# Performance work log

Hardware: AMD Instinct MI355X
Metric: run time of the kernel (lower is better)

Reference implementation:

```python
import jax, jax.numpy as jnp
import numpy as np

D_MODEL = 1024
NUM_HEADS = 16
HEAD_DIM = D_MODEL // NUM_HEADS  # 64
B, S = 4, 2048


def setup_inputs() -> dict:
    key = jax.random.key(0)
    ks = jax.random.split(key, 10)
    scale = 1.0 / np.sqrt(D_MODEL)
    x = jax.random.normal(ks[0], (B, S, D_MODEL), dtype=jnp.float32)
    # per-head projection weights stacked over the head axis (matches ModuleList of Linears)
    Wq = jax.random.normal(ks[1], (NUM_HEADS, D_MODEL, HEAD_DIM), dtype=jnp.float32) * scale
    bq = jax.random.normal(ks[2], (NUM_HEADS, HEAD_DIM), dtype=jnp.float32) * 0.01
    Wk = jax.random.normal(ks[3], (NUM_HEADS, D_MODEL, HEAD_DIM), dtype=jnp.float32) * scale
    bk = jax.random.normal(ks[4], (NUM_HEADS, HEAD_DIM), dtype=jnp.float32) * 0.01
    Wv = jax.random.normal(ks[5], (NUM_HEADS, D_MODEL, HEAD_DIM), dtype=jnp.float32) * scale
    bv = jax.random.normal(ks[6], (NUM_HEADS, HEAD_DIM), dtype=jnp.float32) * 0.01
    Wo = jax.random.normal(ks[7], (D_MODEL, D_MODEL), dtype=jnp.float32) * scale
    bo = jax.random.normal(ks[8], (D_MODEL,), dtype=jnp.float32) * 0.01
    return {"hidden_state": x, "Wq": Wq, "bq": bq, "Wk": Wk, "bk": bk,
            "Wv": Wv, "bv": bv, "Wo": Wo, "bo": bo}


def reference(hidden_state, Wq, bq, Wk, bk, Wv, bv, Wo, bo):
    # q,k,v: [B, H, S, E]
    q = jnp.einsum('bsd,hde->bhse', hidden_state, Wq) + bq[None, :, None, :]
    k = jnp.einsum('bsd,hde->bhse', hidden_state, Wk) + bk[None, :, None, :]
    v = jnp.einsum('bsd,hde->bhse', hidden_state, Wv) + bv[None, :, None, :]
    scores = jnp.einsum('bhse,bhte->bhst', q, k) / jnp.sqrt(jnp.asarray(HEAD_DIM, q.dtype))
    weights = jax.nn.softmax(scores, axis=-1)  # [B, H, S, S]
    attn = jnp.einsum('bhst,bhte->bhse', weights, v)  # [B, H, S, E]
    # concat heads along feature dim (head order preserved)
    attn = jnp.transpose(attn, (0, 2, 1, 3)).reshape(hidden_state.shape[0], hidden_state.shape[1], D_MODEL)
    return attn @ Wo + bo
```

## Files before the change

### kernel.cpp

```cpp
#include <hip/hip_runtime.h>

typedef __bf16 bf16x8 __attribute__((ext_vector_type(8)));
typedef float f32x4 __attribute__((ext_vector_type(4)));
typedef unsigned int u32x4 __attribute__((ext_vector_type(4)));
typedef unsigned int u32x2 __attribute__((ext_vector_type(2)));
typedef unsigned short u16x8 __attribute__((ext_vector_type(8)));

#define MFMA_BF16(a, b, c) __builtin_amdgcn_mfma_f32_16x16x32_bf16((a), (b), (c), 0, 0, 0)

#define QSCALE 0.18033688011112043f

__device__ __forceinline__ unsigned short f2bf(float f) {
    unsigned int u = __builtin_bit_cast(unsigned int, f);
    u += 0x7FFFu + ((u >> 16) & 1u);
    return (unsigned short)(u >> 16);
}

__device__ __forceinline__ unsigned int pack_bf16_rne(float a, float b) {
    unsigned int ua = __builtin_bit_cast(unsigned int, a);
    unsigned int ub = __builtin_bit_cast(unsigned int, b);
    ua += 0x7FFFu + ((ua >> 16) & 1u);
    ub += 0x7FFFu + ((ub >> 16) & 1u);
    return __builtin_amdgcn_perm(ub, ua, 0x07060302);
}

#if __has_builtin(__builtin_amdgcn_cvt_pk_bf16_f32)
typedef __bf16 bf16x2 __attribute__((ext_vector_type(2)));
__device__ __forceinline__ unsigned int pack_bf16(float a, float b) {
    return __builtin_bit_cast(unsigned int, __builtin_amdgcn_cvt_pk_bf16_f32(a, b));
}
#else
__device__ __forceinline__ unsigned int pack_bf16(float a, float b) {
    return pack_bf16_rne(a, b);
}
#endif

#if __has_builtin(__builtin_amdgcn_exp2f)
__device__ __forceinline__ float fast_exp2(float x) { return __builtin_amdgcn_exp2f(x); }
#else
__device__ __forceinline__ float fast_exp2(float x) { return exp2f(x); }
#endif

__device__ __forceinline__ bf16x8 ldfrag(const unsigned short* p) {
    return __builtin_bit_cast(bf16x8, *(const u32x4*)p);
}

typedef const __attribute__((address_space(1))) void* gas_t;
typedef __attribute__((address_space(3))) void* las_t;
__device__ __forceinline__ void dma16(const unsigned short* g, unsigned short* l) {
    __builtin_amdgcn_global_load_lds((gas_t)(const void*)g, (las_t)(void*)l, 16, 0, 0);
}

__device__ __forceinline__ void pipeline_barrier() {
    __builtin_amdgcn_s_waitcnt(0);
    __syncthreads();
}


__global__ void cvt_x_kernel(const float* __restrict__ in, unsigned short* __restrict__ out) {
    long long t = (long long)blockIdx.x * 256 + threadIdx.x;
    const f32x4* p = (const f32x4*)in + t * 2;
    f32x4 v0 = p[0], v1 = p[1];
    u16x8 o;
    o[0] = f2bf(v0[0]); o[1] = f2bf(v0[1]); o[2] = f2bf(v0[2]); o[3] = f2bf(v0[3]);
    o[4] = f2bf(v1[0]); o[5] = f2bf(v1[1]); o[6] = f2bf(v1[2]); o[7] = f2bf(v1[3]);
    *((u16x8*)out + t) = o;
}

__global__ void cvt_wqkvT_kernel(const float* __restrict__ Wq, const float* __restrict__ Wk,
                                 const float* __restrict__ Wv, unsigned short* __restrict__ WT) {
    int n = blockIdx.x * 256 + threadIdx.x;
    int d0 = blockIdx.y * 8;
    int proj = n >> 10, rem = n & 1023, h = rem >> 6, e = rem & 63;
    const float* W = (proj == 0) ? Wq : (proj == 1) ? Wk : Wv;
    const float* src = W + (size_t)h * 65536 + (size_t)d0 * 64 + e;
    u16x8 o;
#pragma unroll
    for (int j = 0; j < 8; j++) o[j] = f2bf(src[j * 64]);
    *(u16x8*)(WT + (size_t)n * 1024 + d0) = o;
}

__global__ void cvt_woT_kernel(const float* __restrict__ Wo, unsigned short* __restrict__ WoT) {
    int n = blockIdx.x * 256 + threadIdx.x;
    int d0 = blockIdx.y * 8;
    const float* src = Wo + (size_t)d0 * 1024 + n;
    u16x8 o;
#pragma unroll
    for (int j = 0; j < 8; j++) o[j] = f2bf(src[j * 1024]);
    *(u16x8*)(WoT + (size_t)n * 1024 + d0) = o;
}


__global__ __launch_bounds__(256) void gemm_qkv_kernel(
    const unsigned short* __restrict__ A, const unsigned short* __restrict__ BT,
    const float* __restrict__ bq, const float* __restrict__ bk, const float* __restrict__ bv,
    unsigned short* __restrict__ Qo, unsigned short* __restrict__ Ko, unsigned short* __restrict__ VTo) {
    __shared__ unsigned short As[2 * 128 * 32];
    __shared__ unsigned short Bs[2 * 128 * 32];
    const int tid = threadIdx.x;
    const int m0 = blockIdx.y * 128, n0 = blockIdx.x * 128;
    const int w = tid >> 6, lane = tid & 63, lr = lane & 15, quad = lane >> 4;
    const int wy = w >> 1, wx = w & 1;
    f32x4 acc[4][4];
#pragma unroll
    for (int i = 0; i < 4; i++)
#pragma unroll
        for (int j = 0; j < 4; j++) acc[i][j] = (f32x4){0.f, 0.f, 0.f, 0.f};
    const int drow = lane >> 2;
    const int dchunk = (lane & 3) ^ (drow & 3);
    const unsigned short* gA = A + (size_t)(m0 + w * 32 + drow) * 1024 + dchunk * 8;
    const unsigned short* gB = BT + (size_t)(n0 + w * 32 + drow) * 1024 + dchunk * 8;
    const int swav = (w * 32) * 32;
    const int fcol = (quad ^ (lr & 3)) * 8;
    dma16(gA, As + swav);
    dma16(gA + 16 * 1024, As + swav + 16 * 32);
    dma16(gB, Bs + swav);
    dma16(gB + 16 * 1024, Bs + swav + 16 * 32);
    for (int k0 = 0; k0 < 1024; k0 += 32) {
        const int cur = (k0 >> 5) & 1;
        const unsigned short* cA = As + cur * 4096;
        const unsigned short* cB = Bs + cur * 4096;
        pipeline_barrier();
        bf16x8 af[4], bfr[4];
#pragma unroll
        for (int i = 0; i < 4; i++) af[i] = ldfrag(cA + (wy * 64 + i * 16 + lr) * 32 + fcol);
#pragma unroll
        for (int j = 0; j < 4; j++) bfr[j] = ldfrag(cB + (wx * 64 + j * 16 + lr) * 32 + fcol);
        if (k0 + 32 < 1024) {
            const int nb = (cur ^ 1) * 4096 + swav;
            dma16(gA + k0 + 32, As + nb);
            dma16(gA + k0 + 32 + 16 * 1024, As + nb + 16 * 32);
            dma16(gB + k0 + 32, Bs + nb);
            dma16(gB + k0 + 32 + 16 * 1024, Bs + nb + 16 * 32);
        }
#pragma unroll
        for (int i = 0; i < 4; i++)
#pragma unroll
            for (int j = 0; j < 4; j++) acc[i][j] = MFMA_BF16(af[i], bfr[j], acc[i][j]);
    }
#pragma unroll
    for (int j = 0; j < 4; j++) {
        int n = n0 + wx * 64 + j * 16 + lr;
        int proj = n >> 10, rem = n & 1023, h = rem >> 6, e = rem & 63;
        if (proj == 2) {
            float bb = bv[rem];
#pragma unroll
            for (int i = 0; i < 4; i++) {
                int m = m0 + wy * 64 + i * 16 + quad * 4;
                int batch = m >> 11, s = m & 2047;
                u32x2 pk;
                pk[0] = pack_bf16_rne(acc[i][j][0] + bb, acc[i][j][1] + bb);
                pk[1] = pack_bf16_rne(acc[i][j][2] + bb, acc[i][j][3] + bb);
                *(u32x2*)(VTo + (((size_t)batch * 16 + h) * 64 + e) * 2048 + s) = pk;
            }
        } else {
            const float* bias = (proj == 0) ? bq : bk;
            unsigned short* dst = (proj == 0) ? Qo : Ko;
            float bb = bias[rem];
            float scl = (proj == 0) ? QSCALE : 1.0f;
#pragma unroll
            for (int i = 0; i < 4; i++) {
#pragma unroll
                for (int r = 0; r < 4; r++) {
                    int m = m0 + wy * 64 + i * 16 + quad * 4 + r;
                    int batch = m >> 11, s = m & 2047;
                    dst[(((size_t)batch * 16 + h) * 2048 + s) * 64 + e] = f2bf((acc[i][j][r] + bb) * scl);
                }
            }
        }
    }
}

__global__ __launch_bounds__(256) void gemm_out_kernel(
    const unsigned short* __restrict__ A, const unsigned short* __restrict__ BT,
    const float* __restrict__ bo, float* __restrict__ out) {
    __shared__ unsigned short As[2 * 128 * 32];
    __shared__ unsigned short Bs[2 * 128 * 32];
    const int tid = threadIdx.x;
    const int m0 = blockIdx.y * 128, n0 = blockIdx.x * 128;
    const int w = tid >> 6, lane = tid & 63, lr = lane & 15, quad = lane >> 4;
    const int wy = w >> 1, wx = w & 1;
    f32x4 acc[4][4];
#pragma unroll
    for (int i = 0; i < 4; i++)
#pragma unroll
        for (int j = 0; j < 4; j++) acc[i][j] = (f32x4){0.f, 0.f, 0.f, 0.f};
    const int drow = lane >> 2;
    const int dchunk = (lane & 3) ^ (drow & 3);
    const unsigned short* gA = A + (size_t)(m0 + w * 32 + drow) * 1024 + dchunk * 8;
    const unsigned short* gB = BT + (size_t)(n0 + w * 32 + drow) * 1024 + dchunk * 8;
    const int swav = (w * 32) * 32;
    const int fcol = (quad ^ (lr & 3)) * 8;
    dma16(gA, As + swav);
    dma16(gA + 16 * 1024, As + swav + 16 * 32);
    dma16(gB, Bs + swav);
    dma16(gB + 16 * 1024, Bs + swav + 16 * 32);
    for (int k0 = 0; k0 < 1024; k0 += 32) {
        const int cur = (k0 >> 5) & 1;
        const unsigned short* cA = As + cur * 4096;
        const unsigned short* cB = Bs + cur * 4096;
        pipeline_barrier();
        bf16x8 af[4], bfr[4];
#pragma unroll
        for (int i = 0; i < 4; i++) af[i] = ldfrag(cA + (wy * 64 + i * 16 + lr) * 32 + fcol);
#pragma unroll
        for (int j = 0; j < 4; j++) bfr[j] = ldfrag(cB + (wx * 64 + j * 16 + lr) * 32 + fcol);
        if (k0 + 32 < 1024) {
            const int nb = (cur ^ 1) * 4096 + swav;
            dma16(gA + k0 + 32, As + nb);
            dma16(gA + k0 + 32 + 16 * 1024, As + nb + 16 * 32);
            dma16(gB + k0 + 32, Bs + nb);
            dma16(gB + k0 + 32 + 16 * 1024, Bs + nb + 16 * 32);
        }
#pragma unroll
        for (int i = 0; i < 4; i++)
#pragma unroll
            for (int j = 0; j < 4; j++) acc[i][j] = MFMA_BF16(af[i], bfr[j], acc[i][j]);
    }
#pragma unroll
    for (int j = 0; j < 4; j++) {
        int n = n0 + wx * 64 + j * 16 + lr;
        float bb = bo[n];
#pragma unroll
        for (int i = 0; i < 4; i++) {
#pragma unroll
            for (int r = 0; r < 4; r++) {
                int m = m0 + wy * 64 + i * 16 + quad * 4 + r;
                out[(size_t)m * 1024 + n] = acc[i][j][r] + bb;
            }
        }
    }
}

#define ST 72
__global__ __launch_bounds__(256) void attn_fa_kernel(
    const unsigned short* __restrict__ Q, const unsigned short* __restrict__ K,
    const unsigned short* __restrict__ VT, unsigned short* __restrict__ Out) {
    __shared__ unsigned short Ks[2 * 64 * 64];
    __shared__ unsigned short Vs[2 * 64 * 64];
    __shared__ unsigned short Ps[128 * ST];
    const int bh = blockIdx.y;
    const int q0 = blockIdx.x * 128;
    const int tid = threadIdx.x;
    const int w = tid >> 6, lane = tid & 63, lr = lane & 15, quad = lane >> 4;
    const unsigned short* Qh = Q + (size_t)bh * 2048 * 64;
    const unsigned short* Kh = K + (size_t)bh * 2048 * 64;
    const unsigned short* Vh = VT + (size_t)bh * 64 * 2048;

    const int drow = lane >> 3;
    const int dchunk = (lane & 7) ^ drow;
    const unsigned short* gK = Kh + (size_t)(w * 16 + drow) * 64 + dchunk * 8;
    const unsigned short* gV = Vh + (size_t)(w * 16 + drow) * 2048 + dchunk * 8;
    const int swav = (w * 16) * 64;
    dma16(gK, Ks + swav);
    dma16(gK + 8 * 64, Ks + swav + 8 * 64);
    dma16(gV, Vs + swav);
    dma16(gV + 8 * 2048, Vs + swav + 8 * 64);

    {
        int r = tid >> 1, c = (tid & 1) * 32;
        const unsigned short* g = Qh + (size_t)(q0 + r) * 64 + c;
        unsigned short* s = Ps + r * ST + c;
        *(u32x4*)s = *(const u32x4*)g;
        *(u32x4*)(s + 8) = *(const u32x4*)(g + 8);
        *(u32x4*)(s + 16) = *(const u32x4*)(g + 16);
        *(u32x4*)(s + 24) = *(const u32x4*)(g + 24);
    }
    bf16x8 qb[2][2];
#pragma unroll
    for (int nt = 0; nt < 2; nt++)
#pragma unroll
        for (int kc = 0; kc < 2; kc++)
            qb[nt][kc] = ldfrag(Ps + (w * 32 + nt * 16 + lr) * ST + kc * 32 + quad * 8);

    f32x4 o[2][4];
#pragma unroll
    for (int i = 0; i < 2; i++)
#pragma unroll
        for (int j = 0; j < 4; j++) o[i][j] = (f32x4){0.f, 0.f, 0.f, 0.f};
    float lp[2] = {0.f, 0.f};

    for (int t0 = 0; t0 < 2048; t0 += 64) {
        const int cur = (t0 >> 6) & 1;
        const unsigned short* cK = Ks + cur * 4096;
        const unsigned short* cV = Vs + cur * 4096;
        pipeline_barrier();
        bf16x8 ka[2][4], vb[2][4];
#pragma unroll
        for (int kc = 0; kc < 2; kc++)
#pragma unroll
            for (int mt = 0; mt < 4; mt++) {
                int fc = ((kc * 4 + quad) ^ (lr & 7)) * 8;
                ka[kc][mt] = ldfrag(cK + (mt * 16 + lr) * 64 + fc);
                vb[kc][mt] = ldfrag(cV + (mt * 16 + lr) * 64 + fc);
            }
        if (t0 + 64 < 2048) {
            const int nb = (cur ^ 1) * 4096 + swav;
            dma16(gK + (size_t)(t0 + 64) * 64, Ks + nb);
            dma16(gK + (size_t)(t0 + 64) * 64 + 8 * 64, Ks + nb + 8 * 64);
            dma16(gV + t0 + 64, Vs + nb);
            dma16(gV + t0 + 64 + 8 * 2048, Vs + nb + 8 * 64);
        }

        f32x4 sc[4][2];
#pragma unroll
        for (int mt = 0; mt < 4; mt++) {
            sc[mt][0] = (f32x4){0.f, 0.f, 0.f, 0.f};
            sc[mt][1] = (f32x4){0.f, 0.f, 0.f, 0.f};
        }
#pragma unroll
        for (int kc = 0; kc < 2; kc++)
#pragma unroll
            for (int mt = 0; mt < 4; mt++) {
                sc[mt][0] = MFMA_BF16(ka[kc][mt], qb[0][kc], sc[mt][0]);
                sc[mt][1] = MFMA_BF16(ka[kc][mt], qb[1][kc], sc[mt][1]);
            }

#pragma unroll
        for (int nt = 0; nt < 2; nt++) {
            unsigned short* prow = Ps + (w * 32 + nt * 16 + lr) * ST + quad * 4;
#pragma unroll
            for (int mt = 0; mt < 4; mt++) {
                float p0 = fast_exp2(sc[mt][nt][0]);
                float p1 = fast_exp2(sc[mt][nt][1]);
                float p2 = fast_exp2(sc[mt][nt][2]);
                float p3 = fast_exp2(sc[mt][nt][3]);
                lp[nt] += (p0 + p1) + (p2 + p3);
                u32x2 pk;
                pk[0] = pack_bf16(p0, p1);
                pk[1] = pack_bf16(p2, p3);
                *(u32x2*)(prow + mt * 16) = pk;
            }
        }

#pragma unroll
        for (int kc = 0; kc < 2; kc++) {
            bf16x8 pa0 = ldfrag(Ps + (w * 32 + lr) * ST + kc * 32 + quad * 8);
            bf16x8 pa1 = ldfrag(Ps + (w * 32 + 16 + lr) * ST + kc * 32 + quad * 8);
#pragma unroll
            for (int et = 0; et < 4; et++) {
                o[0][et] = MFMA_BF16(pa0, vb[kc][et], o[0][et]);
                o[1][et] = MFMA_BF16(pa1, vb[kc][et], o[1][et]);
            }
        }
    }

#pragma unroll
    for (int nt = 0; nt < 2; nt++) {
        float l = lp[nt];
        l += __shfl_xor(l, 16, 64);
        l += __shfl_xor(l, 32, 64);
        lp[nt] = l;
    }

    const int h = bh & 15, b = bh >> 4;
#pragma unroll
    for (int mt = 0; mt < 2; mt++) {
#pragma unroll
        for (int r = 0; r < 4; r++) {
            float l = __shfl(lp[mt], quad * 4 + r, 16);
            float inv = 1.0f / l;
            int s = q0 + w * 32 + mt * 16 + quad * 4 + r;
#pragma unroll
            for (int et = 0; et < 4; et++) {
                int col = h * 64 + et * 16 + lr;
                Out[((size_t)(b * 2048 + s)) * 1024 + col] = f2bf(o[mt][et][r] * inv);
            }
        }
    }
}


extern "C" void kernel_launch(void* const* d_in, const int* in_sizes, int n_in,
                              void* d_out, int out_size, void* d_ws, size_t ws_size,
                              hipStream_t stream) {
    const float* x  = (const float*)d_in[0];
    const float* Wq = (const float*)d_in[1];
    const float* bq = (const float*)d_in[2];
    const float* Wk = (const float*)d_in[3];
    const float* bk = (const float*)d_in[4];
    const float* Wv = (const float*)d_in[5];
    const float* bv = (const float*)d_in[6];
    const float* Wo = (const float*)d_in[7];
    const float* bo = (const float*)d_in[8];
    float* out = (float*)d_out;

    char* ws = (char*)d_ws;
    unsigned short* xb    = (unsigned short*)(ws);
    unsigned short* WqkvT = (unsigned short*)(ws + 16777216);
    unsigned short* WoT   = (unsigned short*)(ws + 23068672);
    unsigned short* Qb    = (unsigned short*)(ws + 25165824);
    unsigned short* Kb    = (unsigned short*)(ws + 41943040);
    unsigned short* VTb   = (unsigned short*)(ws + 58720256);
    unsigned short* attn  = xb;

    cvt_x_kernel<<<dim3(4096), dim3(256), 0, stream>>>(x, xb);
    cvt_wqkvT_kernel<<<dim3(12, 128), dim3(256), 0, stream>>>(Wq, Wk, Wv, WqkvT);
    cvt_woT_kernel<<<dim3(4, 128), dim3(256), 0, stream>>>(Wo, WoT);
    gemm_qkv_kernel<<<dim3(24, 64), dim3(256), 0, stream>>>(xb, WqkvT, bq, bk, bv, Qb, Kb, VTb);
    attn_fa_kernel<<<dim3(16, 64), dim3(256), 0, stream>>>(Qb, Kb, VTb, attn);
    gemm_out_kernel<<<dim3(8, 64), dim3(256), 0, stream>>>(attn, WoT, bo, out);
}
```

Before: 299.9 us.

## Double attention query tile per block and swizzle P tile in LDS

The flash-attention kernel now has each wave handle 64 query rows instead of 32, so each block covers 256 queries. Every K/V tile loaded into LDS is therefore reused across twice as many queries, halving K/V traffic per query. The padded P buffer is replaced by an XOR-swizzled 64-wide layout, Q fragments are read straight from global memory, and V fragments are loaded per k-chunk to ease register pressure. The grid is reordered with heads on the x axis and launch bounds request two blocks per CU. The costs are more registers per thread for accumulators and half as many blocks in flight (512).

```diff
diff --git a/kernel.cpp b/kernel.cpp
--- a/kernel.cpp
+++ b/kernel.cpp
@@ -232,20 +232,21 @@
     }
 }
 
-#define ST 72
-__global__ __launch_bounds__(256) void attn_fa_kernel(
+__global__ __launch_bounds__(256, 2) void attn_fa_kernel(
     const unsigned short* __restrict__ Q, const unsigned short* __restrict__ K,
     const unsigned short* __restrict__ VT, unsigned short* __restrict__ Out) {
     __shared__ unsigned short Ks[2 * 64 * 64];
     __shared__ unsigned short Vs[2 * 64 * 64];
-    __shared__ unsigned short Ps[128 * ST];
-    const int bh = blockIdx.y;
-    const int q0 = blockIdx.x * 128;
+    __shared__ unsigned short Ps[256 * 64];
+    const int bh = blockIdx.x;
+    const int q0 = blockIdx.y * 256;
     const int tid = threadIdx.x;
     const int w = tid >> 6, lane = tid & 63, lr = lane & 15, quad = lane >> 4;
     const unsigned short* Qh = Q + (size_t)bh * 2048 * 64;
     const unsigned short* Kh = K + (size_t)bh * 2048 * 64;
     const unsigned short* Vh = VT + (size_t)bh * 64 * 2048;
+
+    const f32x4 ZERO4 = {0.f, 0.f, 0.f, 0.f};
 
     const int drow = lane >> 3;
     const int dchunk = (lane & 7) ^ drow;
@@ -257,43 +258,34 @@
     dma16(gV, Vs + swav);
     dma16(gV + 8 * 2048, Vs + swav + 8 * 64);
 
-    {
-        int r = tid >> 1, c = (tid & 1) * 32;
-        const unsigned short* g = Qh + (size_t)(q0 + r) * 64 + c;
-        unsigned short* s = Ps + r * ST + c;
-        *(u32x4*)s = *(const u32x4*)g;
-        *(u32x4*)(s + 8) = *(const u32x4*)(g + 8);
-        *(u32x4*)(s + 16) = *(const u32x4*)(g + 16);
-        *(u32x4*)(s + 24) = *(const u32x4*)(g + 24);
-    }
-    bf16x8 qb[2][2];
-#pragma unroll
-    for (int nt = 0; nt < 2; nt++)
+    bf16x8 qb[4][2];
+#pragma unroll
+    for (int nt = 0; nt < 4; nt++)
 #pragma unroll
         for (int kc = 0; kc < 2; kc++)
-            qb[nt][kc] = ldfrag(Ps + (w * 32 + nt * 16 + lr) * ST + kc * 32 + quad * 8);
-
-    f32x4 o[2][4];
-#pragma unroll
-    for (int i = 0; i < 2; i++)
-#pragma unroll
-        for (int j = 0; j < 4; j++) o[i][j] = (f32x4){0.f, 0.f, 0.f, 0.f};
-    float lp[2] = {0.f, 0.f};
+            qb[nt][kc] = ldfrag(Qh + (size_t)(q0 + w * 64 + nt * 16 + lr) * 64 + kc * 32 + quad * 8);
+
+    f32x4 o[4][4];
+#pragma unroll
+    for (int i = 0; i < 4; i++)
+#pragma unroll
+        for (int j = 0; j < 4; j++) o[i][j] = ZERO4;
+    float lp[4] = {0.f, 0.f, 0.f, 0.f};
+
+    unsigned short* const Pw = Ps + (w * 64) * 64;
+    const int swzb = lr & 7;
 
     for (int t0 = 0; t0 < 2048; t0 += 64) {
         const int cur = (t0 >> 6) & 1;
         const unsigned short* cK = Ks + cur * 4096;
         const unsigned short* cV = Vs + cur * 4096;
         pipeline_barrier();
-        bf16x8 ka[2][4], vb[2][4];
+        bf16x8 ka[2][4];
 #pragma unroll
         for (int kc = 0; kc < 2; kc++)
 #pragma unroll
-            for (int mt = 0; mt < 4; mt++) {
-                int fc = ((kc * 4 + quad) ^ (lr & 7)) * 8;
-                ka[kc][mt] = ldfrag(cK + (mt * 16 + lr) * 64 + fc);
-                vb[kc][mt] = ldfrag(cV + (mt * 16 + lr) * 64 + fc);
-            }
+            for (int mt = 0; mt < 4; mt++)
+                ka[kc][mt] = ldfrag(cK + (mt * 16 + lr) * 64 + ((kc * 4 + quad) ^ swzb) * 8);
         if (t0 + 64 < 2048) {
             const int nb = (cur ^ 1) * 4096 + swav;
             dma16(gK + (size_t)(t0 + 64) * 64, Ks + nb);
@@ -302,69 +294,67 @@
             dma16(gV + t0 + 64 + 8 * 2048, Vs + nb + 8 * 64);
         }
 
-        f32x4 sc[4][2];
 #pragma unroll
         for (int mt = 0; mt < 4; mt++) {
-            sc[mt][0] = (f32x4){0.f, 0.f, 0.f, 0.f};
-            sc[mt][1] = (f32x4){0.f, 0.f, 0.f, 0.f};
-        }
-#pragma unroll
-        for (int kc = 0; kc < 2; kc++)
-#pragma unroll
-            for (int mt = 0; mt < 4; mt++) {
-                sc[mt][0] = MFMA_BF16(ka[kc][mt], qb[0][kc], sc[mt][0]);
-                sc[mt][1] = MFMA_BF16(ka[kc][mt], qb[1][kc], sc[mt][1]);
-            }
-
-#pragma unroll
-        for (int nt = 0; nt < 2; nt++) {
-            unsigned short* prow = Ps + (w * 32 + nt * 16 + lr) * ST + quad * 4;
-#pragma unroll
-            for (int mt = 0; mt < 4; mt++) {
-                float p0 = fast_exp2(sc[mt][nt][0]);
-                float p1 = fast_exp2(sc[mt][nt][1]);
-                float p2 = fast_exp2(sc[mt][nt][2]);
-                float p3 = fast_exp2(sc[mt][nt][3]);
+            f32x4 sc[4];
+#pragma unroll
+            for (int nt = 0; nt < 4; nt++) {
+                f32x4 z = ZERO4;
+                sc[nt] = MFMA_BF16(ka[0][mt], qb[nt][0], z);
+                sc[nt] = MFMA_BF16(ka[1][mt], qb[nt][1], sc[nt]);
+            }
+#pragma unroll
+            for (int nt = 0; nt < 4; nt++) {
+                float p0 = fast_exp2(sc[nt][0]);
+                float p1 = fast_exp2(sc[nt][1]);
+                float p2 = fast_exp2(sc[nt][2]);
+                float p3 = fast_exp2(sc[nt][3]);
                 lp[nt] += (p0 + p1) + (p2 + p3);
                 u32x2 pk;
                 pk[0] = pack_bf16(p0, p1);
                 pk[1] = pack_bf16(p2, p3);
-                *(u32x2*)(prow + mt * 16) = pk;
+                *(u32x2*)(Pw + (nt * 16 + lr) * 64 + ((2 * mt + (quad >> 1)) ^ swzb) * 8 +
+                          (quad & 1) * 4) = pk;
             }
         }
 
 #pragma unroll
         for (int kc = 0; kc < 2; kc++) {
-            bf16x8 pa0 = ldfrag(Ps + (w * 32 + lr) * ST + kc * 32 + quad * 8);
-            bf16x8 pa1 = ldfrag(Ps + (w * 32 + 16 + lr) * ST + kc * 32 + quad * 8);
-#pragma unroll
-            for (int et = 0; et < 4; et++) {
-                o[0][et] = MFMA_BF16(pa0, vb[kc][et], o[0][et]);
-                o[1][et] = MFMA_BF16(pa1, vb[kc][et], o[1][et]);
-            }
-        }
-    }
-
-#pragma unroll
-    for (int nt = 0; nt < 2; nt++) {
-        float l = lp[nt];
+            const int fc = ((kc * 4 + quad) ^ swzb) * 8;
+            bf16x8 vb[4];
+#pragma unroll
+            for (int et = 0; et < 4; et++) vb[et] = ldfrag(cV + (et * 16 + lr) * 64 + fc);
+#pragma unroll
+            for (int g = 0; g < 4; g++) {
+                bf16x8 pa = ldfrag(Pw + (g * 16 + lr) * 64 + fc);
+                o[g][0] = MFMA_BF16(pa, vb[0], o[g][0]);
+                o[g][1] = MFMA_BF16(pa, vb[1], o[g][1]);
+                o[g][2] = MFMA_BF16(pa, vb[2], o[g][2]);
+                o[g][3] = MFMA_BF16(pa, vb[3], o[g][3]);
+            }
+        }
+    }
+
+#pragma unroll
+    for (int g = 0; g < 4; g++) {
+        float l = lp[g];
         l += __shfl_xor(l, 16, 64);
         l += __shfl_xor(l, 32, 64);
-        lp[nt] = l;
+        lp[g] = l;
     }
 
     const int h = bh & 15, b = bh >> 4;
 #pragma unroll
-    for (int mt = 0; mt < 2; mt++) {
+    for (int g = 0; g < 4; g++) {
 #pragma unroll
         for (int r = 0; r < 4; r++) {
-            float l = __shfl(lp[mt], quad * 4 + r, 16);
+            float l = __shfl(lp[g], quad * 4 + r, 16);
             float inv = 1.0f / l;
-            int s = q0 + w * 32 + mt * 16 + quad * 4 + r;
+            int s = q0 + w * 64 + g * 16 + quad * 4 + r;
 #pragma unroll
             for (int et = 0; et < 4; et++) {
                 int col = h * 64 + et * 16 + lr;
-                Out[((size_t)(b * 2048 + s)) * 1024 + col] = f2bf(o[mt][et][r] * inv);
+                Out[((size_t)(b * 2048 + s)) * 1024 + col] = f2bf(o[g][et][r] * inv);
             }
         }
     }
@@ -398,6 +388,6 @@
     cvt_wqkvT_kernel<<<dim3(12, 128), dim3(256), 0, stream>>>(Wq, Wk, Wv, WqkvT);
     cvt_woT_kernel<<<dim3(4, 128), dim3(256), 0, stream>>>(Wo, WoT);
     gemm_qkv_kernel<<<dim3(24, 64), dim3(256), 0, stream>>>(xb, WqkvT, bq, bk, bv, Qb, Kb, VTb);
-    attn_fa_kernel<<<dim3(16, 64), dim3(256), 0, stream>>>(Qb, Kb, VTb, attn);
+    attn_fa_kernel<<<dim3(64, 8), dim3(256), 0, stream>>>(Qb, Kb, VTb, attn);
     gemm_out_kernel<<<dim3(8, 64), dim3(256), 0, stream>>>(attn, WoT, bo, out);
 }
```

New measurement: 281.8 us. -6.0%, faster.
